# Kernel optimization log

Hardware: AMD Instinct MI355X
Metric: run time of the kernel (lower is better)

Reference implementation:

```python
import jax, jax.numpy as jnp
import numpy as np

N_EMBED = 1024
N_HEADS = 16
HEAD_DIM = N_EMBED // N_HEADS


def setup_inputs() -> dict:
    key = jax.random.key(0)
    ks = jax.random.split(key, 5)
    x = jax.random.normal(ks[0], (4, 2048, N_EMBED), dtype=jnp.float32)
    # Linear params stored as [in, out] (y = x @ W + b), math-equivalent to torch Linear
    scale_attn = 1.0 / np.sqrt(N_EMBED)
    W_attn = jax.random.normal(ks[1], (N_EMBED, 3 * N_EMBED), dtype=jnp.float32) * scale_attn
    b_attn = jax.random.normal(ks[2], (3 * N_EMBED,), dtype=jnp.float32) * 0.02
    W_proj = jax.random.normal(ks[3], (N_EMBED, N_EMBED), dtype=jnp.float32) * scale_attn
    b_proj = jax.random.normal(ks[4], (N_EMBED,), dtype=jnp.float32) * 0.02
    return {"x": x, "W_attn": W_attn, "b_attn": b_attn, "W_proj": W_proj, "b_proj": b_proj}


def reference(x, W_attn, b_attn, W_proj, b_proj):
    BS, SL, ED = x.shape
    qkv = x @ W_attn + b_attn                      # [B, S, 3E]
    q, k, v = jnp.split(qkv, 3, axis=2)
    # [B, H, S, D]
    def heads(t):
        return t.reshape(BS, SL, N_HEADS, HEAD_DIM).transpose(0, 2, 1, 3)
    q, k, v = heads(q), heads(k), heads(v)
    att = jnp.einsum('bhqd,bhkd->bhqk', q, k) * (HEAD_DIM ** -0.5)
    causal = jnp.tril(jnp.ones((SL, SL), dtype=bool))
    att = jnp.where(causal[None, None], att, -jnp.inf)
    att = jax.nn.softmax(att, axis=-1)
    y = jnp.einsum('bhqk,bhkd->bhqd', att, v)      # [B, H, S, D]
    y = y.transpose(0, 2, 1, 3).reshape(BS, SL, ED)
    return y @ W_proj + b_proj
```

## Files before the change

### kernel.cpp

```cpp
#include <hip/hip_runtime.h>


#define BATCH 4
#define SEQ   2048
#define EMB   1024
#define NH    16
#define HD    64

typedef __bf16 bf16;
typedef __bf16 bf16x8 __attribute__((ext_vector_type(8)));
typedef float  f32x4  __attribute__((ext_vector_type(4)));

__device__ __forceinline__ void ld_lds16(const void* g, void* l) {
  __builtin_amdgcn_global_load_lds(
      (const __attribute__((address_space(1))) void*)g,
      (__attribute__((address_space(3))) void*)l, 16, 0, 0);
}

__global__ void cvt_f32_bf16(const float* __restrict__ in, bf16* __restrict__ out, int n) {
  int i = (blockIdx.x * blockDim.x + threadIdx.x) * 4;
  if (i + 3 < n) {
    float4 v = *(const float4*)(in + i);
    bf16 o0 = (bf16)v.x, o1 = (bf16)v.y, o2 = (bf16)v.z, o3 = (bf16)v.w;
    out[i] = o0; out[i+1] = o1; out[i+2] = o2; out[i+3] = o3;
  }
}

__global__ void transpose_cvt2(const float* __restrict__ Wa, const float* __restrict__ Wp,
                               bf16* __restrict__ WaT, bf16* __restrict__ WpT) {
  __shared__ float tile[32][33];
  int bx = blockIdx.x;
  const float* W; bf16* WT; int N;
  if (bx < 96) { W = Wa; WT = WaT; N = 3072; }
  else         { W = Wp; WT = WpT; N = 1024; bx -= 96; }
  int n0 = bx * 32, k0 = blockIdx.y * 32;
  int tx = threadIdx.x & 31, ty = threadIdx.x >> 5;
#pragma unroll
  for (int r = 0; r < 4; r++) {
    int k = k0 + ty + r * 8;
    tile[ty + r * 8][tx] = W[(long)k * N + n0 + tx];
  }
  __syncthreads();
#pragma unroll
  for (int r = 0; r < 4; r++) {
    int n = n0 + ty + r * 8;
    WT[(long)n * EMB + k0 + tx] = (bf16)tile[tx][ty + r * 8];
  }
}

#define QSCALE 0.18033688f

template <int BNT>
__global__ __launch_bounds__(256, 3) void gemm_bt(
    const bf16* __restrict__ A, const bf16* __restrict__ Bt,
    const float* __restrict__ bias, int Kdim, int Ncols, int mode,
    bf16* __restrict__ q, bf16* __restrict__ k, bf16* __restrict__ v,
    float* __restrict__ out)
{
  constexpr int NF = BNT / 32;
  __shared__ __align__(16) bf16 Al[128 * 64];
  __shared__ __align__(16) bf16 Bl[BNT * 64];
  int lin = blockIdx.x;
  int xcd = lin & 7, s = lin >> 3;
  int bx = s >> 3, by = xcd * 8 + (s & 7);
  int m0 = by * 128;
  int n0 = bx * BNT;
  int t = threadIdx.x;
  int wave = t >> 6, lane = t & 63;
  int l15 = lane & 15, quad = lane >> 4;
  int wm = (wave & 1) * 64, wn = (wave >> 1) * (BNT / 2);

  f32x4 acc[4][NF] = {};

  for (int kt = 0; kt < Kdim; kt += 64) {
    __syncthreads();
#pragma unroll
    for (int it = 0; it < 4; ++it) {
      int c = it * 256 + t;
      int row = c >> 3, u = c & 7;
      ld_lds16(&A[(long)(m0 + row) * Kdim + kt + ((u ^ (row & 7)) * 8)],
               &Al[(it * 256 + wave * 64) * 8]);
    }
#pragma unroll
    for (int it = 0; it < BNT / 32; ++it) {
      int c = it * 256 + t;
      int row = c >> 3, u = c & 7;
      ld_lds16(&Bt[(long)(n0 + row) * Kdim + kt + ((u ^ (row & 7)) * 8)],
               &Bl[(it * 256 + wave * 64) * 8]);
    }
    __syncthreads();
#pragma unroll
    for (int ks = 0; ks < 2; ++ks) {
      bf16x8 af[4], bfr[NF];
#pragma unroll
      for (int i = 0; i < 4; ++i) {
        int r = wm + i * 16 + l15;
        af[i] = *(const bf16x8*)(&Al[r * 64 + (((ks * 4 + quad) ^ (r & 7)) * 8)]);
      }
#pragma unroll
      for (int i = 0; i < NF; ++i) {
        int r = wn + i * 16 + l15;
        bfr[i] = *(const bf16x8*)(&Bl[r * 64 + (((ks * 4 + quad) ^ (r & 7)) * 8)]);
      }
#pragma unroll
      for (int mi = 0; mi < 4; ++mi)
#pragma unroll
        for (int ni = 0; ni < NF; ++ni)
          acc[mi][ni] = __builtin_amdgcn_mfma_f32_16x16x32_bf16(af[mi], bfr[ni], acc[mi][ni], 0, 0, 0);
    }
  }

#pragma unroll
  for (int mi = 0; mi < 4; ++mi) {
#pragma unroll
    for (int ni = 0; ni < NF; ++ni) {
      int gcol = n0 + wn + ni * 16 + l15;
      float bv = bias[gcol];
#pragma unroll
      for (int i = 0; i < 4; ++i) {
        int grow = m0 + wm + mi * 16 + quad * 4 + i;
        float val = acc[mi][ni][i] + bv;
        if (mode == 0) {
          int which = gcol >> 10, e = gcol & 1023;
          int h = e >> 6, d = e & 63;
          int b = grow >> 11, ss = grow & 2047;
          if (which == 0) {
            q[(((long)b * NH + h) * SEQ + ss) * HD + d] = (bf16)(val * QSCALE);
          } else if (which == 1) {
            k[(((long)b * NH + h) * SEQ + ss) * HD + d] = (bf16)val;
          } else {
            v[(((long)b * NH + h) * HD + d) * SEQ + ss] = (bf16)val;
          }
        } else {
          out[(long)grow * Ncols + gcol] = val;
        }
      }
    }
  }
}

#define LDP 72

__global__ __launch_bounds__(256, 2) void attn(
    const bf16* __restrict__ Q, const bf16* __restrict__ K,
    const bf16* __restrict__ Vt, bf16* __restrict__ Y)
{
  __shared__ __align__(16) bf16 Kl[64 * 64];
  __shared__ __align__(16) bf16 Vl[64 * 64];
  __shared__ __align__(16) bf16 Pl[4][32 * LDP];
  int L = blockIdx.x;
  int a = L >> 3;
  int hd = (L & 7) + 8 * (a & 7);
  int st = a >> 3;
  int b = hd >> 4, h = hd & 15;
  const bf16* Qp  = Q  + (((long)b * NH + h) * SEQ) * HD;
  const bf16* Kp  = K  + (((long)b * NH + h) * SEQ) * HD;
  const bf16* Vtp = Vt + (((long)b * NH + h) * HD) * SEQ;
  int t = threadIdx.x, wave = t >> 6, lane = t & 63;
  int l15 = lane & 15, quad = lane >> 4;

#pragma unroll 1
  for (int pass = 0; pass < 2; ++pass) {
    int q0 = (pass == 0) ? st * 128 : (SEQ - 128) - st * 128;
    int wq0 = q0 + wave * 32;

    bf16x8 qf[2][2];
#pragma unroll
    for (int m = 0; m < 2; ++m) {
      const bf16* qrow = Qp + (long)(wq0 + m * 16 + l15) * HD + quad * 8;
      qf[m][0] = *(const bf16x8*)(qrow);
      qf[m][1] = *(const bf16x8*)(qrow + 32);
    }
    float lrow[2][4] = {};
    f32x4 oacc[2][4] = {};

    int ntiles = q0 / 64 + 2;
#pragma unroll 1
    for (int kt = 0; kt < ntiles; ++kt) {
      int k0 = kt * 64;
      __syncthreads();
#pragma unroll
      for (int it = 0; it < 2; ++it) {
        int cu = it * 256 + t;
        int row = cu >> 3, u = cu & 7;
        ld_lds16(&Kp[(long)(k0 + row) * HD + ((u ^ (row & 7)) * 8)],
                 &Kl[(it * 256 + wave * 64) * 8]);
        ld_lds16(&Vtp[(long)row * SEQ + k0 + ((u ^ (row & 7)) * 8)],
                 &Vl[(it * 256 + wave * 64) * 8]);
      }
      __syncthreads();
      if (k0 > wq0 + 31) continue;

      f32x4 sc[2][4] = {};
#pragma unroll
      for (int kk = 0; kk < 2; ++kk) {
#pragma unroll
        for (int ni = 0; ni < 4; ++ni) {
          int r = ni * 16 + l15, u = kk * 4 + quad;
          bf16x8 kfr = *(const bf16x8*)(&Kl[r * 64 + ((u ^ (r & 7)) * 8)]);
          sc[0][ni] = __builtin_amdgcn_mfma_f32_16x16x32_bf16(qf[0][kk], kfr, sc[0][ni], 0, 0, 0);
          sc[1][ni] = __builtin_amdgcn_mfma_f32_16x16x32_bf16(qf[1][kk], kfr, sc[1][ni], 0, 0, 0);
        }
      }

      bool full = (k0 + 63 <= wq0);
#pragma unroll
      for (int m = 0; m < 2; ++m) {
#pragma unroll
        for (int i = 0; i < 4; ++i) {
          int qr = wq0 + m * 16 + quad * 4 + i;
          float e[4];
#pragma unroll
          for (int ni = 0; ni < 4; ++ni) {
            float x = sc[m][ni][i];
            if (!full) x = (k0 + ni * 16 + l15 <= qr) ? x : -1e30f;
            e[ni] = __builtin_amdgcn_exp2f(x);
          }
          lrow[m][i] += (e[0] + e[1]) + (e[2] + e[3]);
          int prow = (m * 16 + quad * 4 + i) * LDP;
#pragma unroll
          for (int ni = 0; ni < 4; ++ni)
            Pl[wave][prow + ni * 16 + l15] = (bf16)e[ni];
        }
      }
      asm volatile("s_waitcnt lgkmcnt(0)" ::: "memory");
#pragma unroll
      for (int kk = 0; kk < 2; ++kk) {
        int kbase = kk * 32 + quad * 8;
        bf16x8 pf0 = *(const bf16x8*)(&Pl[wave][(l15) * LDP + kbase]);
        bf16x8 pf1 = *(const bf16x8*)(&Pl[wave][(16 + l15) * LDP + kbase]);
#pragma unroll
        for (int ni = 0; ni < 4; ++ni) {
          int dd = ni * 16 + l15, u = kk * 4 + quad;
          bf16x8 vf = *(const bf16x8*)(&Vl[dd * 64 + ((u ^ (dd & 7)) * 8)]);
          oacc[0][ni] = __builtin_amdgcn_mfma_f32_16x16x32_bf16(pf0, vf, oacc[0][ni], 0, 0, 0);
          oacc[1][ni] = __builtin_amdgcn_mfma_f32_16x16x32_bf16(pf1, vf, oacc[1][ni], 0, 0, 0);
        }
      }
    }
#pragma unroll
    for (int m = 0; m < 2; ++m) {
#pragma unroll
      for (int i = 0; i < 4; ++i) {
        float rs = lrow[m][i];
#pragma unroll
        for (int off = 8; off; off >>= 1) rs += __shfl_xor(rs, off, 16);
        float inv = 1.0f / rs;
        int qr = wq0 + m * 16 + quad * 4 + i;
        bf16* dst = Y + ((long)(b * SEQ + qr)) * EMB + h * HD;
#pragma unroll
        for (int ni = 0; ni < 4; ++ni)
          dst[ni * 16 + l15] = (bf16)(oacc[m][ni][i] * inv);
      }
    }
  }
}

extern "C" void kernel_launch(void* const* d_in, const int* in_sizes, int n_in,
                              void* d_out, int out_size, void* d_ws, size_t ws_size,
                              hipStream_t stream) {
  const float* x      = (const float*)d_in[0];
  const float* W_attn = (const float*)d_in[1];
  const float* b_attn = (const float*)d_in[2];
  const float* W_proj = (const float*)d_in[3];
  const float* b_proj = (const float*)d_in[4];
  float* out = (float*)d_out;
  char* ws = (char*)d_ws;
  bf16* xb  = (bf16*)(ws);
  bf16* WaT = (bf16*)(ws + 16777216);
  bf16* WpT = (bf16*)(ws + 23068672);
  bf16* Qb  = (bf16*)(ws + 25165824);
  bf16* Kb  = (bf16*)(ws + 41943040);
  bf16* Vtb = (bf16*)(ws + 58720256);
  bf16* Yb  = (bf16*)(ws + 75497472);

  cvt_f32_bf16<<<8192, 256, 0, stream>>>(x, xb, BATCH * SEQ * EMB);
  transpose_cvt2<<<dim3(128, 32), 256, 0, stream>>>(W_attn, W_proj, WaT, WpT);
  gemm_bt<128><<<1536, 256, 0, stream>>>(xb, WaT, b_attn, EMB, 3 * EMB, 0,
                                         Qb, Kb, Vtb, nullptr);
  attn<<<512, 256, 0, stream>>>(Qb, Kb, Vtb, Yb);
  gemm_bt<64><<<1024, 256, 0, stream>>>(Yb, WpT, b_proj, EMB, EMB, 1,
                                        nullptr, nullptr, nullptr, out);
}
```

Measured before the change: 247.7 us.

## Double-buffer K/V tiles in attention with async prefetch of next tile

```diff
diff --git a/kernel.cpp b/kernel.cpp
--- a/kernel.cpp
+++ b/kernel.cpp
@@ -141,12 +141,12 @@
 
 #define LDP 72
 
-__global__ __launch_bounds__(256, 2) void attn(
+__global__ __launch_bounds__(256, 3) void attn(
     const bf16* __restrict__ Q, const bf16* __restrict__ K,
     const bf16* __restrict__ Vt, bf16* __restrict__ Y)
 {
-  __shared__ __align__(16) bf16 Kl[64 * 64];
-  __shared__ __align__(16) bf16 Vl[64 * 64];
+  __shared__ __align__(16) bf16 Kl[2][64 * 64];
+  __shared__ __align__(16) bf16 Vl[2][64 * 64];
   __shared__ __align__(16) bf16 Pl[4][32 * LDP];
   int L = blockIdx.x;
   int a = L >> 3;
@@ -158,6 +158,7 @@
   const bf16* Vtp = Vt + (((long)b * NH + h) * HD) * SEQ;
   int t = threadIdx.x, wave = t >> 6, lane = t & 63;
   int l15 = lane & 15, quad = lane >> 4;
+  int srow = t >> 3, su = t & 7;
 
 #pragma unroll 1
   for (int pass = 0; pass < 2; ++pass) {
@@ -175,68 +176,89 @@
     f32x4 oacc[2][4] = {};
 
     int ntiles = q0 / 64 + 2;
+
+    {
+      int k0 = 0;
+#pragma unroll
+      for (int it = 0; it < 2; ++it) {
+        int row = it * 32 + srow;
+        ld_lds16(&Kp[(long)(k0 + row) * HD + ((su ^ (row & 7)) * 8)],
+                 &Kl[0][(it * 256 + wave * 64) * 8]);
+        ld_lds16(&Vtp[(long)row * SEQ + k0 + ((su ^ (row & 7)) * 8)],
+                 &Vl[0][(it * 256 + wave * 64) * 8]);
+      }
+    }
+
 #pragma unroll 1
     for (int kt = 0; kt < ntiles; ++kt) {
       int k0 = kt * 64;
-      __syncthreads();
-#pragma unroll
-      for (int it = 0; it < 2; ++it) {
-        int cu = it * 256 + t;
-        int row = cu >> 3, u = cu & 7;
-        ld_lds16(&Kp[(long)(k0 + row) * HD + ((u ^ (row & 7)) * 8)],
-                 &Kl[(it * 256 + wave * 64) * 8]);
-        ld_lds16(&Vtp[(long)row * SEQ + k0 + ((u ^ (row & 7)) * 8)],
-                 &Vl[(it * 256 + wave * 64) * 8]);
-      }
-      __syncthreads();
-      if (k0 > wq0 + 31) continue;
-
-      f32x4 sc[2][4] = {};
-#pragma unroll
-      for (int kk = 0; kk < 2; ++kk) {
-#pragma unroll
-        for (int ni = 0; ni < 4; ++ni) {
-          int r = ni * 16 + l15, u = kk * 4 + quad;
-          bf16x8 kfr = *(const bf16x8*)(&Kl[r * 64 + ((u ^ (r & 7)) * 8)]);
-          sc[0][ni] = __builtin_amdgcn_mfma_f32_16x16x32_bf16(qf[0][kk], kfr, sc[0][ni], 0, 0, 0);
-          sc[1][ni] = __builtin_amdgcn_mfma_f32_16x16x32_bf16(qf[1][kk], kfr, sc[1][ni], 0, 0, 0);
-        }
-      }
-
-      bool full = (k0 + 63 <= wq0);
-#pragma unroll
-      for (int m = 0; m < 2; ++m) {
-#pragma unroll
-        for (int i = 0; i < 4; ++i) {
-          int qr = wq0 + m * 16 + quad * 4 + i;
-          float e[4];
+      if (kt + 1 < ntiles) {
+        int k0n = k0 + 64, nb = (kt + 1) & 1;
+#pragma unroll
+        for (int it = 0; it < 2; ++it) {
+          int row = it * 32 + srow;
+          ld_lds16(&Kp[(long)(k0n + row) * HD + ((su ^ (row & 7)) * 8)],
+                   &Kl[nb][(it * 256 + wave * 64) * 8]);
+          ld_lds16(&Vtp[(long)row * SEQ + k0n + ((su ^ (row & 7)) * 8)],
+                   &Vl[nb][(it * 256 + wave * 64) * 8]);
+        }
+        asm volatile("s_waitcnt vmcnt(4)" ::: "memory");
+      } else {
+        asm volatile("s_waitcnt vmcnt(0)" ::: "memory");
+      }
+      asm volatile("s_barrier" ::: "memory");
+
+      const bf16* Kc = Kl[kt & 1];
+      const bf16* Vc = Vl[kt & 1];
+      if (k0 <= wq0 + 31) {
+        f32x4 sc[2][4] = {};
+#pragma unroll
+        for (int kk = 0; kk < 2; ++kk) {
 #pragma unroll
           for (int ni = 0; ni < 4; ++ni) {
-            float x = sc[m][ni][i];
-            if (!full) x = (k0 + ni * 16 + l15 <= qr) ? x : -1e30f;
-            e[ni] = __builtin_amdgcn_exp2f(x);
+            int r = ni * 16 + l15, u = kk * 4 + quad;
+            bf16x8 kfr = *(const bf16x8*)(&Kc[r * 64 + ((u ^ (r & 7)) * 8)]);
+            sc[0][ni] = __builtin_amdgcn_mfma_f32_16x16x32_bf16(qf[0][kk], kfr, sc[0][ni], 0, 0, 0);
+            sc[1][ni] = __builtin_amdgcn_mfma_f32_16x16x32_bf16(qf[1][kk], kfr, sc[1][ni], 0, 0, 0);
           }
-          lrow[m][i] += (e[0] + e[1]) + (e[2] + e[3]);
-          int prow = (m * 16 + quad * 4 + i) * LDP;
-#pragma unroll
-          for (int ni = 0; ni < 4; ++ni)
-            Pl[wave][prow + ni * 16 + l15] = (bf16)e[ni];
-        }
-      }
-      asm volatile("s_waitcnt lgkmcnt(0)" ::: "memory");
-#pragma unroll
-      for (int kk = 0; kk < 2; ++kk) {
-        int kbase = kk * 32 + quad * 8;
-        bf16x8 pf0 = *(const bf16x8*)(&Pl[wave][(l15) * LDP + kbase]);
-        bf16x8 pf1 = *(const bf16x8*)(&Pl[wave][(16 + l15) * LDP + kbase]);
-#pragma unroll
-        for (int ni = 0; ni < 4; ++ni) {
-          int dd = ni * 16 + l15, u = kk * 4 + quad;
-          bf16x8 vf = *(const bf16x8*)(&Vl[dd * 64 + ((u ^ (dd & 7)) * 8)]);
-          oacc[0][ni] = __builtin_amdgcn_mfma_f32_16x16x32_bf16(pf0, vf, oacc[0][ni], 0, 0, 0);
-          oacc[1][ni] = __builtin_amdgcn_mfma_f32_16x16x32_bf16(pf1, vf, oacc[1][ni], 0, 0, 0);
-        }
-      }
+        }
+
+        bool full = (k0 + 63 <= wq0);
+#pragma unroll
+        for (int m = 0; m < 2; ++m) {
+#pragma unroll
+          for (int i = 0; i < 4; ++i) {
+            int qr = wq0 + m * 16 + quad * 4 + i;
+            float e[4];
+#pragma unroll
+            for (int ni = 0; ni < 4; ++ni) {
+              float x = sc[m][ni][i];
+              if (!full) x = (k0 + ni * 16 + l15 <= qr) ? x : -1e30f;
+              e[ni] = __builtin_amdgcn_exp2f(x);
+            }
+            lrow[m][i] += (e[0] + e[1]) + (e[2] + e[3]);
+            int prow = (m * 16 + quad * 4 + i) * LDP;
+#pragma unroll
+            for (int ni = 0; ni < 4; ++ni)
+              Pl[wave][prow + ni * 16 + l15] = (bf16)e[ni];
+          }
+        }
+        asm volatile("s_waitcnt lgkmcnt(0)" ::: "memory");
+#pragma unroll
+        for (int kk = 0; kk < 2; ++kk) {
+          int kbase = kk * 32 + quad * 8;
+          bf16x8 pf0 = *(const bf16x8*)(&Pl[wave][(l15) * LDP + kbase]);
+          bf16x8 pf1 = *(const bf16x8*)(&Pl[wave][(16 + l15) * LDP + kbase]);
+#pragma unroll
+          for (int ni = 0; ni < 4; ++ni) {
+            int dd = ni * 16 + l15, u = kk * 4 + quad;
+            bf16x8 vf = *(const bf16x8*)(&Vc[dd * 64 + ((u ^ (dd & 7)) * 8)]);
+            oacc[0][ni] = __builtin_amdgcn_mfma_f32_16x16x32_bf16(pf0, vf, oacc[0][ni], 0, 0, 0);
+            oacc[1][ni] = __builtin_amdgcn_mfma_f32_16x16x32_bf16(pf1, vf, oacc[1][ni], 0, 0, 0);
+          }
+        }
+      }
+      asm volatile("s_barrier" ::: "memory");
     }
 #pragma unroll
     for (int m = 0; m < 2; ++m) {
```

Measured after the change: 257.9 us. 1.04x slower.
